# Kernel tuning notes

Measured on AMD Instinct MI355X. Metric: run time of the kernel, lower is better.

The kernel has to match this reference:

```python
import jax, jax.numpy as jnp
import numpy as np

# module hyperparameters (match init_kwargs)
D_IN = 32
N_BAND_IN = 32
D_OUT = 32
K_BAND = 4
K_T = 3
DIL_T = 1
STRIDE_B = 2
PAD_B = 1
PAD_B_OUT = 0

# derived band geometry (same formulas as ConvTranspose2dBandPadder)
N_UP = (N_BAND_IN - 1) * STRIDE_B + 1            # zero-interleaved bands
PAD_TOP = K_BAND - 1 - PAD_B
PAD_BOT = PAD_TOP + PAD_B_OUT
N_PADDED = N_UP + PAD_TOP + PAD_BOT              # bands fed to the conv
N_BAND_OUT = N_PADDED - K_BAND + 1               # valid conv along bands

B = 8
T = 1000


def setup_inputs() -> dict:
    key = jax.random.key(0)
    k1, k2, k3 = jax.random.split(key, 3)
    x = jax.random.normal(k1, (B, D_IN * N_BAND_IN, T), jnp.float32)
    W = jax.random.normal(k2, (D_OUT, D_IN, K_BAND, K_T), jnp.float32) * 0.05
    b = jax.random.normal(k3, (D_OUT,), jnp.float32) * 0.05
    return {"x": x, "W": W, "b": b}


def reference(x, W, b):
    """x: (B, D_IN*N_BAND_IN, T) band-major channels -> (B, D_OUT*N_BAND_OUT, T)."""
    Bs, _, Ts = x.shape
    # chunk(dim=1, n_band_in): band-major layout (band, feature)
    bands = x.reshape(Bs, N_BAND_IN, D_IN, Ts)
    # zero-interleave bands by stride + top/bottom zero-band padding
    up = jnp.zeros((Bs, N_PADDED, D_IN, Ts), x.dtype)
    up = up.at[:, PAD_TOP:PAD_TOP + N_UP:STRIDE_B].set(bands)
    # 2D conv: channels = D_IN, spatial = (band, time), causal in time
    xin = up.transpose(0, 2, 1, 3)  # (B, D_IN, N_PADDED, T)
    pad_t = (K_T - 1) * DIL_T
    y = jax.lax.conv_general_dilated(
        xin, W,
        window_strides=(1, 1),
        padding=((0, 0), (pad_t, 0)),  # valid over bands, causal over time
        rhs_dilation=(1, DIL_T),
        dimension_numbers=("NCHW", "OIHW", "NCHW"),
    )  # (B, D_OUT, N_BAND_OUT, T)
    y = y + b[None, :, None, None]
    # back to band-major flattened channels
    return y.transpose(0, 2, 1, 3).reshape(Bs, D_OUT * N_BAND_OUT, Ts)
```

## Files before the change

kernel.cpp:

```cpp
#include <hip/hip_runtime.h>
#include <cstddef>
#include <cstdint>


typedef __bf16 bf16x8 __attribute__((ext_vector_type(8)));
typedef __bf16 bf16x4 __attribute__((ext_vector_type(4)));
typedef float  f32x4  __attribute__((ext_vector_type(4)));

#define D_IN_ 32
#define D_OUT_ 32
#define N_BI_ 32
#define N_BO_ 64
#define K_B_ 4
#define K_T_ 3
#define T_ 1000
#define B_ 8

#define TT_ 500
#define XR_ 512
#define ROWB_ 64
#define WT_ELEMS (2 * 6 * 2 * 64 * 8)

__device__ __forceinline__ int swz(int t) { return (t & 3) ^ ((t >> 2) & 3); }

__global__ __launch_bounds__(256)
void wprep(const float* __restrict__ W, __bf16* __restrict__ wt) {
    int idx = blockIdx.x * 256 + threadIdx.x;
    if (idx >= WT_ELEMS) return;
    int r = idx & 7, l = (idx >> 3) & 63, mt = (idx >> 9) & 1, rest = idx >> 10;
    int ks = rest % 6, p = rest / 6;
    int dout = mt * 16 + (l & 15), din = (l >> 4) * 8 + r;
    int j = ks / 3, kt = ks % 3, kb = 2 * j + p;
    wt[idx] = (__bf16)W[((dout * D_IN_ + din) * K_B_ + kb) * K_T_ + kt];
}

__global__ __launch_bounds__(512, 2)
void tct_pair(const float* __restrict__ x, const __bf16* __restrict__ wt,
              const float* __restrict__ bias, float* __restrict__ out)
{
    __shared__ unsigned char xl[2 * XR_ * ROWB_];

    const int wg  = blockIdx.x;
    const int bb  = wg & 7;
    const int rr  = wg >> 3;
    const int kk  = rr >> 1;
    const int th  = rr & 1;
    const int k   = kk - 1;
    const int t0  = th * TT_;

    const int tid = threadIdx.x;
    const int l   = tid & 63;
    const int w   = tid >> 6;
    const int mt  = w >> 2;
    const int wq  = w & 3;
    const int tl  = l & 15;
    const int cch = l >> 4;

    {
        const int g  = tid >> 4;
        const int u  = tid & 15;
        const int si = u >> 3;
        const int dg = u & 7;
        const int s  = k + si;
        const bool bandok = (s >= 0) && (s < N_BI_);
        const float* xb = x + ((size_t)(bb * N_BI_ + (bandok ? s : 0)) * D_IN_ + dg * 4) * T_;
        unsigned char* lbase = xl + si * (XR_ * ROWB_);
        const int c = dg >> 1, h = dg & 1;

        f32x4 vv[4][4];
#pragma unroll
        for (int it = 0; it < 4; ++it) {
            const int tg = t0 - 4 + (g + it * 32) * 4;
            const bool ok = bandok && (tg >= 0) && (tg < T_);
#pragma unroll
            for (int i = 0; i < 4; ++i)
                vv[it][i] = ok ? *(const f32x4*)(xb + (size_t)i * T_ + tg)
                               : (f32x4){0.f, 0.f, 0.f, 0.f};
        }
#pragma unroll
        for (int it = 0; it < 4; ++it) {
            const int tq = g + it * 32;
#pragma unroll
            for (int e = 0; e < 4; ++e) {
                const int t = tq * 4 + e;
                bf16x4 row;
                row[0] = (__bf16)vv[it][0][e];
                row[1] = (__bf16)vv[it][1][e];
                row[2] = (__bf16)vv[it][2][e];
                row[3] = (__bf16)vv[it][3][e];
                *(bf16x4*)(lbase + t * ROWB_ + ((c ^ swz(t)) << 4) + (h << 3)) = row;
            }
        }
    }

    bf16x8 afrag[2][6];
    {
        const bf16x8* wp = (const bf16x8*)wt;
#pragma unroll
        for (int p = 0; p < 2; ++p)
#pragma unroll
            for (int ks = 0; ks < 6; ++ks)
                afrag[p][ks] = wp[p * 768 + ks * 128 + mt * 64 + l];
    }

    const int dout = mt * 16 + tl;
    const float bvs = bias[dout];

    __syncthreads();

#pragma unroll
    for (int ntc = 0; ntc < 2; ++ntc) {
        f32x4 acc[2][4];
#pragma unroll
        for (int p = 0; p < 2; ++p)
#pragma unroll
            for (int n4 = 0; n4 < 4; ++n4)
#pragma unroll
                for (int r = 0; r < 4; ++r) acc[p][n4][r] = 0.f;

#pragma unroll
        for (int n4 = 0; n4 < 4; ++n4) {
            const int nt = ntc * 4 + n4;
#pragma unroll
            for (int j = 0; j < 2; ++j) {
                const unsigned char* xbnd = xl + j * (XR_ * ROWB_);
#pragma unroll
                for (int kt = 0; kt < 3; ++kt) {
                    const int lt = (wq * 128 + nt * 16 + tl + kt + 2) & (XR_ - 1);
                    const bf16x8 xfrag = *(const bf16x8*)(xbnd + lt * ROWB_
                                                          + ((cch ^ swz(lt)) << 4));
                    const int ks = j * 3 + kt;
                    acc[0][n4] = __builtin_amdgcn_mfma_f32_16x16x32_bf16(xfrag, afrag[0][ks], acc[0][n4], 0, 0, 0);
                    acc[1][n4] = __builtin_amdgcn_mfma_f32_16x16x32_bf16(xfrag, afrag[1][ks], acc[1][n4], 0, 0, 0);
                }
            }
        }

#pragma unroll
        for (int p = 0; p < 2; ++p) {
            const int n = 2 * k + 2 - p;
            if (n < 0 || n >= N_BO_) continue;
            float* opb = out + ((size_t)(bb * N_BO_ + n) * D_OUT_ + dout) * T_;
#pragma unroll
            for (int n4 = 0; n4 < 4; ++n4) {
                const int lcol = wq * 128 + (ntc * 4 + n4) * 16 + cch * 4;
                if (lcol < TT_) {
                    f32x4 v = acc[p][n4];
                    v[0] += bvs; v[1] += bvs; v[2] += bvs; v[3] += bvs;
                    *(f32x4*)(opb + t0 + lcol) = v;
                }
            }
        }
    }
}

__global__ __launch_bounds__(256)
void tct_fallback(const float* __restrict__ x, const float* __restrict__ W,
                  const float* __restrict__ bias, float* __restrict__ out)
{
    const int lane = threadIdx.x & 63;
    const int wav  = __builtin_amdgcn_readfirstlane(threadIdx.x >> 6);
    const int dog  = wav * 8;
    const int n    = blockIdx.y;
    const int bb   = blockIdx.z;
    const int p    = n & 1;
    int t0 = blockIdx.x * 256 + lane * 4;
    const bool act = (t0 < T_);
    if (!act) t0 = T_ - 4;
    float acc[8][4];
#pragma unroll
    for (int i = 0; i < 8; ++i)
#pragma unroll
        for (int u = 0; u < 4; ++u) acc[i][u] = 0.f;
#pragma unroll
    for (int j = 0; j < 2; ++j) {
        const int s = (n + 2 * j + p - 2) >> 1;
        if (s < 0 || s >= N_BI_) continue;
        const int kb = 2 * j + p;
        const float* xband = x + (size_t)(bb * N_BI_ + s) * D_IN_ * T_;
        for (int d_in = 0; d_in < D_IN_; ++d_in) {
            const float* xr = xband + d_in * T_;
            const float4 xc = *(const float4*)(xr + t0);
            float4 xp = make_float4(0.f, 0.f, 0.f, 0.f);
            if (t0 > 0) xp = *(const float4*)(xr + t0 - 4);
            const float xv[6] = {xp.z, xp.w, xc.x, xc.y, xc.z, xc.w};
#pragma unroll
            for (int kt = 0; kt < K_T_; ++kt) {
                float wv[8];
#pragma unroll
                for (int i = 0; i < 8; ++i) {
                    const int widx = __builtin_amdgcn_readfirstlane(
                        (((dog + i) * D_IN_ + d_in) * K_B_ + kb) * K_T_ + kt);
                    wv[i] = W[widx];
                }
#pragma unroll
                for (int i = 0; i < 8; ++i)
#pragma unroll
                    for (int u = 0; u < 4; ++u)
                        acc[i][u] = fmaf(wv[i], xv[u + kt], acc[i][u]);
            }
        }
    }
    if (act) {
        float bvv[8];
#pragma unroll
        for (int i = 0; i < 8; ++i) bvv[i] = bias[dog + i];
        float* op = out + ((size_t)(bb * N_BO_ + n) * D_OUT_ + dog) * T_ + t0;
#pragma unroll
        for (int i = 0; i < 8; ++i) {
            float4 v;
            v.x = acc[i][0] + bvv[i]; v.y = acc[i][1] + bvv[i];
            v.z = acc[i][2] + bvv[i]; v.w = acc[i][3] + bvv[i];
            *(float4*)(op + (size_t)i * T_) = v;
        }
    }
}

extern "C" void kernel_launch(void* const* d_in, const int* in_sizes, int n_in,
                              void* d_out, int out_size, void* d_ws, size_t ws_size,
                              hipStream_t stream) {
    const float* x    = (const float*)d_in[0];
    const float* W    = (const float*)d_in[1];
    const float* bias = (const float*)d_in[2];
    float* out = (float*)d_out;

    if (ws_size >= (size_t)WT_ELEMS * sizeof(__bf16)) {
        __bf16* wt = (__bf16*)d_ws;
        wprep<<<(WT_ELEMS + 255) / 256, 256, 0, stream>>>(W, wt);
        tct_pair<<<dim3(8 * 33 * 2), dim3(512), 0, stream>>>(x, wt, bias, out);
    } else {
        tct_fallback<<<dim3((T_ + 255) / 256, N_BO_, B_), dim3(256), 0, stream>>>(x, W, bias, out);
    }
}
```

Before: 106.5 us.

## Process full time axis per workgroup and fold band-0 output into k=0 blocks

Each workgroup now covers the full 1000-step time range for one (batch, band-pair) instead of half, so the grid drops from 528 to 256 blocks and LDS doubles to 128 KB. The separate k=-1 boundary blocks are removed: blocks with k=0 compute output band 0 with an extra MFMA chain reusing the band-0 fragments. The aim is to cut the duplicate halo loads and the launch of nearly-empty boundary blocks. The risk is that 256 blocks at 128 KB LDS each may fill the CUs poorly (likely one block per CU), and the ntc loop is no longer unrolled.

After: 109.6 us. 1.03x slower.

```diff
diff --git a/kernel.cpp b/kernel.cpp
--- a/kernel.cpp
+++ b/kernel.cpp
@@ -16,9 +16,9 @@
 #define T_ 1000
 #define B_ 8
 
-#define TT_ 500
-#define XR_ 512
+#define XR_ 1024
 #define ROWB_ 64
+#define BANDSTR_ (XR_ * ROWB_)
 #define WT_ELEMS (2 * 6 * 2 * 64 * 8)
 
 __device__ __forceinline__ int swz(int t) { return (t & 3) ^ ((t >> 2) & 3); }
@@ -35,18 +35,14 @@
 }
 
 __global__ __launch_bounds__(512, 2)
-void tct_pair(const float* __restrict__ x, const __bf16* __restrict__ wt,
+void tct_full(const float* __restrict__ x, const __bf16* __restrict__ wt,
               const float* __restrict__ bias, float* __restrict__ out)
 {
-    __shared__ unsigned char xl[2 * XR_ * ROWB_];
+    __shared__ unsigned char xl[2 * BANDSTR_];
 
     const int wg  = blockIdx.x;
     const int bb  = wg & 7;
-    const int rr  = wg >> 3;
-    const int kk  = rr >> 1;
-    const int th  = rr & 1;
-    const int k   = kk - 1;
-    const int t0  = th * TT_;
+    const int k   = wg >> 3;
 
     const int tid = threadIdx.x;
     const int l   = tid & 63;
@@ -62,33 +58,34 @@
         const int si = u >> 3;
         const int dg = u & 7;
         const int s  = k + si;
-        const bool bandok = (s >= 0) && (s < N_BI_);
+        const bool bandok = (s < N_BI_);
         const float* xb = x + ((size_t)(bb * N_BI_ + (bandok ? s : 0)) * D_IN_ + dg * 4) * T_;
-        unsigned char* lbase = xl + si * (XR_ * ROWB_);
+        unsigned char* lbase = xl + si * BANDSTR_;
         const int c = dg >> 1, h = dg & 1;
 
-        f32x4 vv[4][4];
-#pragma unroll
-        for (int it = 0; it < 4; ++it) {
-            const int tg = t0 - 4 + (g + it * 32) * 4;
-            const bool ok = bandok && (tg >= 0) && (tg < T_);
-#pragma unroll
-            for (int i = 0; i < 4; ++i)
-                vv[it][i] = ok ? *(const f32x4*)(xb + (size_t)i * T_ + tg)
-                               : (f32x4){0.f, 0.f, 0.f, 0.f};
-        }
-#pragma unroll
-        for (int it = 0; it < 4; ++it) {
-            const int tq = g + it * 32;
-#pragma unroll
-            for (int e = 0; e < 4; ++e) {
-                const int t = tq * 4 + e;
-                bf16x4 row;
-                row[0] = (__bf16)vv[it][0][e];
-                row[1] = (__bf16)vv[it][1][e];
-                row[2] = (__bf16)vv[it][2][e];
-                row[3] = (__bf16)vv[it][3][e];
-                *(bf16x4*)(lbase + t * ROWB_ + ((c ^ swz(t)) << 4) + (h << 3)) = row;
+        for (int seg = 0; seg < 2; ++seg) {
+            f32x4 vv[4][4];
+#pragma unroll
+            for (int it = 0; it < 4; ++it) {
+                const int tg = seg * 512 + (g + it * 32) * 4 - 4;
+                const bool ok = bandok && (tg >= 0) && (tg < T_);
+#pragma unroll
+                for (int i = 0; i < 4; ++i)
+                    vv[it][i] = ok ? *(const f32x4*)(xb + (size_t)i * T_ + tg)
+                                   : (f32x4){0.f, 0.f, 0.f, 0.f};
+            }
+#pragma unroll
+            for (int it = 0; it < 4; ++it) {
+#pragma unroll
+                for (int e = 0; e < 4; ++e) {
+                    const int r = seg * 512 + (g + it * 32) * 4 + e;
+                    bf16x4 row;
+                    row[0] = (__bf16)vv[it][0][e];
+                    row[1] = (__bf16)vv[it][1][e];
+                    row[2] = (__bf16)vv[it][2][e];
+                    row[3] = (__bf16)vv[it][3][e];
+                    *(bf16x4*)(lbase + r * ROWB_ + ((c ^ swz(r)) << 4) + (h << 3)) = row;
+                }
             }
         }
     }
@@ -105,33 +102,37 @@
 
     const int dout = mt * 16 + tl;
     const float bvs = bias[dout];
+    const bool isk0 = (k == 0);
 
     __syncthreads();
 
-#pragma unroll
-    for (int ntc = 0; ntc < 2; ++ntc) {
+    for (int ntc = 0; ntc < 4; ++ntc) {
         f32x4 acc[2][4];
-#pragma unroll
-        for (int p = 0; p < 2; ++p)
-#pragma unroll
-            for (int n4 = 0; n4 < 4; ++n4)
-#pragma unroll
-                for (int r = 0; r < 4; ++r) acc[p][n4][r] = 0.f;
+        f32x4 acc0[4];
+#pragma unroll
+        for (int n4 = 0; n4 < 4; ++n4) {
+#pragma unroll
+            for (int r = 0; r < 4; ++r) {
+                acc[0][n4][r] = 0.f; acc[1][n4][r] = 0.f; acc0[n4][r] = 0.f;
+            }
+        }
 
 #pragma unroll
         for (int n4 = 0; n4 < 4; ++n4) {
             const int nt = ntc * 4 + n4;
 #pragma unroll
             for (int j = 0; j < 2; ++j) {
-                const unsigned char* xbnd = xl + j * (XR_ * ROWB_);
+                const unsigned char* xbnd = xl + j * BANDSTR_;
 #pragma unroll
                 for (int kt = 0; kt < 3; ++kt) {
-                    const int lt = (wq * 128 + nt * 16 + tl + kt + 2) & (XR_ - 1);
+                    const int lt = (wq * 256 + nt * 16 + tl + kt + 2) & (XR_ - 1);
                     const bf16x8 xfrag = *(const bf16x8*)(xbnd + lt * ROWB_
                                                           + ((cch ^ swz(lt)) << 4));
                     const int ks = j * 3 + kt;
                     acc[0][n4] = __builtin_amdgcn_mfma_f32_16x16x32_bf16(xfrag, afrag[0][ks], acc[0][n4], 0, 0, 0);
                     acc[1][n4] = __builtin_amdgcn_mfma_f32_16x16x32_bf16(xfrag, afrag[1][ks], acc[1][n4], 0, 0, 0);
+                    if (j == 0 && isk0)
+                        acc0[n4] = __builtin_amdgcn_mfma_f32_16x16x32_bf16(xfrag, afrag[0][3 + kt], acc0[n4], 0, 0, 0);
                 }
             }
         }
@@ -139,15 +140,27 @@
 #pragma unroll
         for (int p = 0; p < 2; ++p) {
             const int n = 2 * k + 2 - p;
-            if (n < 0 || n >= N_BO_) continue;
+            if (n >= N_BO_) continue;
             float* opb = out + ((size_t)(bb * N_BO_ + n) * D_OUT_ + dout) * T_;
 #pragma unroll
             for (int n4 = 0; n4 < 4; ++n4) {
-                const int lcol = wq * 128 + (ntc * 4 + n4) * 16 + cch * 4;
-                if (lcol < TT_) {
+                const int lcol = wq * 256 + (ntc * 4 + n4) * 16 + cch * 4;
+                if (lcol < T_) {
                     f32x4 v = acc[p][n4];
                     v[0] += bvs; v[1] += bvs; v[2] += bvs; v[3] += bvs;
-                    *(f32x4*)(opb + t0 + lcol) = v;
+                    *(f32x4*)(opb + lcol) = v;
+                }
+            }
+        }
+        if (isk0) {
+            float* opb = out + ((size_t)(bb * N_BO_ + 0) * D_OUT_ + dout) * T_;
+#pragma unroll
+            for (int n4 = 0; n4 < 4; ++n4) {
+                const int lcol = wq * 256 + (ntc * 4 + n4) * 16 + cch * 4;
+                if (lcol < T_) {
+                    f32x4 v = acc0[n4];
+                    v[0] += bvs; v[1] += bvs; v[2] += bvs; v[3] += bvs;
+                    *(f32x4*)(opb + lcol) = v;
                 }
             }
         }
@@ -227,7 +240,7 @@
     if (ws_size >= (size_t)WT_ELEMS * sizeof(__bf16)) {
         __bf16* wt = (__bf16*)d_ws;
         wprep<<<(WT_ELEMS + 255) / 256, 256, 0, stream>>>(W, wt);
-        tct_pair<<<dim3(8 * 33 * 2), dim3(512), 0, stream>>>(x, wt, bias, out);
+        tct_full<<<dim3(256), dim3(512), 0, stream>>>(x, wt, bias, out);
     } else {
         tct_fallback<<<dim3((T_ + 255) / 256, N_BO_, B_), dim3(256), 0, stream>>>(x, W, bias, out);
     }
```
